# Kernel tuning notes

Hardware: AMD Instinct MI355X
Metric: run time of the kernel (lower is better)

## Reference

```python
import jax, jax.numpy as jnp
import numpy as np
import math

B, S, D, H, DFF, V = 8, 512, 512, 8, 2048, 32000
EPS = 1e-5

def _pe_table(max_len, d):
    pos = jnp.arange(max_len, dtype=jnp.float32)[:, None]
    i = jnp.arange(d)
    exponent = (2 * (i // 2)).astype(jnp.float32) / d
    angle = pos / jnp.power(10000.0, exponent)[None, :]
    return jnp.where(i % 2 == 0, jnp.sin(angle), jnp.cos(angle))

def _ln(x, g, b):
    mu = jnp.mean(x, -1, keepdims=True)
    var = jnp.mean((x - mu) ** 2, -1, keepdims=True)
    return g * (x - mu) * jax.lax.rsqrt(var + EPS) + b

def setup_inputs() -> dict:
    key = jax.random.key(0)
    ks = jax.random.split(key, 16)
    n = jax.random.normal
    return {
        "tokens": jax.random.randint(ks[0], (B, S), 0, V, dtype=jnp.int32),
        "emb": n(ks[1], (V, D), jnp.float32),
        "pe": _pe_table(1000, D),
        "Wq": n(ks[2], (H, D, D), jnp.float32), "bq": jnp.zeros((H, D), jnp.float32),
        "Wk": n(ks[3], (H, D, D), jnp.float32), "bk": jnp.zeros((H, D), jnp.float32),
        "Wv": n(ks[4], (H, D, D), jnp.float32), "bv": jnp.zeros((H, D), jnp.float32),
        "Wo": n(ks[5], (H * D, D), jnp.float32), "bo": jnp.zeros((D,), jnp.float32),
        "g1": jnp.ones((D,), jnp.float32), "be1": jnp.zeros((D,), jnp.float32),
        "W1": n(ks[6], (D, DFF), jnp.float32), "b1": jnp.zeros((DFF,), jnp.float32),
        "W2": n(ks[7], (DFF, D), jnp.float32), "b2": jnp.zeros((D,), jnp.float32),
        "g2": jnp.ones((D,), jnp.float32), "be2": jnp.zeros((D,), jnp.float32),
        "Wf": n(ks[8], (D, V), jnp.float32), "bf": jnp.zeros((V,), jnp.float32),
    }

def reference(tokens, emb, pe, Wq, bq, Wk, bk, Wv, bv, Wo, bo, g1, be1,
              W1, b1, W2, b2, g2, be2, Wf, bf):
    x = emb[tokens] + pe[:tokens.shape[1]]  # [B,S,D]
    res = x
    # input-level "causal" mask over (seq, feature) plane, as in the source
    mask = jnp.triu(jnp.ones((S, D), dtype=bool), k=1)
    xm = jnp.where(mask, 0.0, x)
    scale = 1.0 / math.sqrt(D)
    q = jnp.einsum('bsd,hde->hbse', xm, Wq) + bq[:, None, None, :]
    k = jnp.einsum('bsd,hde->hbse', xm, Wk) + bk[:, None, None, :]
    v = jnp.einsum('bsd,hde->hbse', xm, Wv) + bv[:, None, None, :]
    attn = jax.nn.softmax(jnp.einsum('hbse,hbte->hbst', q, k) * scale, axis=-1)
    o = jnp.einsum('hbst,hbte->hbse', attn, v)  # [H,B,S,D]
    cat = o.transpose(1, 2, 0, 3).reshape(B, S, H * D)  # matches torch.cat head order
    x = _ln(res + (cat @ Wo + bo), g1, be1)
    res = x
    ff = jax.nn.relu(x @ W1 + b1) @ W2 + b2
    x = _ln(res + ff, g2, be2)
    return x @ Wf + bf  # [B,S,V]
```

## Files before the change

kernel.cpp:

```cpp
#include <hip/hip_runtime.h>

typedef unsigned short u16;
typedef unsigned int u32;
typedef short s16x8 __attribute__((ext_vector_type(8)));
typedef __bf16 bf16x8 __attribute__((ext_vector_type(8)));
typedef float f32x4 __attribute__((ext_vector_type(4)));

#define DEVI static __device__ __forceinline__

#define SS 512
#define DD 512
#define NFF 2048
#define VV 32000
#define MTOT 4096
#define HD 4096
#define KC 1536

DEVI float bf2f(u16 h){ return __uint_as_float(((u32)h) << 16); }
DEVI u16 f2bf(float f){
  u32 u = __float_as_uint(f);
  return (u16)((u + 0x7FFFu + ((u >> 16) & 1u)) >> 16);
}
DEVI float ldf(const void* p, long i, int isbf){
  return isbf ? bf2f(((const u16*)p)[i]) : ((const float*)p)[i];
}

DEVI f32x4 mfma16(s16x8 a, s16x8 b, f32x4 c){
  return __builtin_amdgcn_mfma_f32_16x16x32_bf16(
      __builtin_bit_cast(bf16x8, a), __builtin_bit_cast(bf16x8, b), c, 0, 0, 0);
}

typedef const __attribute__((address_space(1))) unsigned int* gup;
typedef __attribute__((address_space(3))) unsigned int* lup;
DEVI void gload16(const void* g, void* l){
  __builtin_amdgcn_global_load_lds((gup)g, (lup)l, 16, 0, 0);
}

DEVI float wave_redsum(float v){
  #pragma unroll
  for (int off = 32; off > 0; off >>= 1) v += __shfl_xor(v, off, 64);
  return v;
}

__global__ void k_dflag(const void* pe, int* flag){
  flag[0] = (*(const u32*)pe == 0x3F800000u) ? 1 : 0;
}

__global__ __launch_bounds__(256) void k_embed(
    const int* __restrict__ tok, const void* __restrict__ emb, const void* __restrict__ pe,
    float* __restrict__ x, u16* __restrict__ xm2, const int* __restrict__ dflag)
{
  int isbf = dflag[0];
  int blk = blockIdx.x;
  int s = blk & (SS - 1);
  int t = tok[blk];
  long rb = (long)blk * 1024;
  for (int d = threadIdx.x; d < DD; d += 256){
    float e = ldf(emb, (long)t * DD + d, isbf) + ldf(pe, (long)s * DD + d, isbf);
    x[(long)blk * DD + d] = e;
    float m = (d <= s) ? e : 0.f;
    u16 hi = f2bf(m);
    u16 lo = f2bf(m - bf2f(hi));
    xm2[rb + d] = hi;
    xm2[rb + 512 + d] = lo;
  }
}

__global__ __launch_bounds__(256) void k_wsplitT(
    const void* __restrict__ Wq, const void* __restrict__ Wk,
    u16* __restrict__ Wq2, u16* __restrict__ Wk2, const int* __restrict__ dflag)
{
  int isbf = dflag[0];
  int zz = blockIdx.z;
  const void* in = (zz < 8) ? Wq : Wk;
  u16* out = (zz < 8) ? Wq2 : Wk2;
  int z = zz & 7;
  long zin = (long)z * DD * DD;
  long zout = (long)z * DD * 1024;
  __shared__ float t[32][33];
  int e0 = blockIdx.x * 32, d0 = blockIdx.y * 32;
  int tx = threadIdx.x & 31, ty = threadIdx.x >> 5;
  #pragma unroll
  for (int i = 0; i < 4; i++){
    int d = ty + i * 8;
    t[d][tx] = ldf(in, zin + (long)(d0 + d) * DD + e0 + tx, isbf);
  }
  __syncthreads();
  #pragma unroll
  for (int i = 0; i < 4; i++){
    int e = ty + i * 8;
    float v = t[tx][e];
    u16 hi = f2bf(v);
    u16 lo = f2bf(v - bf2f(hi));
    long ob = zout + (long)(e0 + e) * 1024 + d0 + tx;
    out[ob] = hi;
    out[ob + 512] = lo;
  }
}

__global__ __launch_bounds__(256) void k_transAll(
    const void* __restrict__ Wv, const void* __restrict__ Wo,
    const void* __restrict__ W1, const void* __restrict__ W2,
    const void* __restrict__ Wf,
    u16* __restrict__ WvT, u16* __restrict__ WoT, u16* __restrict__ W1T,
    u16* __restrict__ W2T, u16* __restrict__ WfT, const int* __restrict__ dflag)
{
  int isbf = dflag[0];
  int f = blockIdx.x;
  const void* in; u16* out; int R, C, gx, loc;
  if (f < 2048)      { in = Wv; out = WvT; R = 512;  C = 512;   gx = 16;   loc = f; }
  else if (f < 4096) { in = Wo; out = WoT; R = 4096; C = 512;   gx = 16;   loc = f - 2048; }
  else if (f < 5120) { in = W1; out = W1T; R = 512;  C = 2048;  gx = 64;   loc = f - 4096; }
  else if (f < 6144) { in = W2; out = W2T; R = 2048; C = 512;   gx = 16;   loc = f - 5120; }
  else               { in = Wf; out = WfT; R = 512;  C = 32000; gx = 1000; loc = f - 6144; }
  int bx = loc % gx;
  int rest = loc / gx;
  int gy = R >> 5;
  int by = rest % gy, z = rest / gy;
  long zo = (long)z * R * C;
  __shared__ float t[32][33];
  int c0 = bx * 32, r0 = by * 32;
  int tx = threadIdx.x & 31, ty = threadIdx.x >> 5;
  #pragma unroll
  for (int i = 0; i < 4; i++){
    int r = ty + i * 8;
    t[r][tx] = ldf(in, zo + (long)(r0 + r) * C + c0 + tx, isbf);
  }
  __syncthreads();
  #pragma unroll
  for (int i = 0; i < 4; i++){
    int c = ty + i * 8;
    out[zo + (long)(c0 + c) * R + r0 + tx] = f2bf(t[tx][c]);
  }
}

enum { EP_QK = 0, EP_SCALE = 1, EP_VT = 2, EP_CAT = 3, EP_OUT = 4,
       EP_F32RES = 5, EP_RELU = 6 };

template<int MODE, bool GSWAP>
__global__ __launch_bounds__(256) void k_mfma(
    const u16* __restrict__ A, long sA, int lda,
    const u16* __restrict__ Bt, long sB,
    void* __restrict__ Cv,
    const void* __restrict__ bias,
    const float* __restrict__ res,
    int K, int ldc, float scale,
    const int* __restrict__ dflag)
{
  int isbf = dflag[0];
  int z = blockIdx.z;
  const u16* Ab = A + (long)z * sA;
  const u16* Bb = Bt + (long)z * sB;
  __shared__ __align__(16) u16 As[2][4][128][8];
  __shared__ __align__(16) u16 Bs[2][4][128][8];
  int m0 = (GSWAP ? blockIdx.x : blockIdx.y) * 128;
  int n0 = (GSWAP ? blockIdx.y : blockIdx.x) * 128;
  int tid = threadIdx.x;
  int lane = tid & 63, w = tid >> 6;
  int wr = (w >> 1) * 64, wc = (w & 1) * 64;
  int l15 = lane & 15, l4 = lane >> 4;
  int s0 = w * 64 + lane;
  int ar0 = s0 & 127, ak0 = s0 >> 7;
  int ak1 = ak0 + 2;
  f32x4 zero = {0.f, 0.f, 0.f, 0.f};
  f32x4 acc[4][4];
  #pragma unroll
  for (int i = 0; i < 4; i++)
    #pragma unroll
    for (int j = 0; j < 4; j++) acc[i][j] = zero;

  const long arow0 = (long)(m0 + ar0) * lda;
  const long brow0 = (long)(n0 + ar0) * K;

  #define STAGE(buf, k0) do{ \
    u16* AsF = &As[buf][0][0][0]; \
    u16* BsF = &Bs[buf][0][0][0]; \
    gload16(Ab + arow0 + (k0) + ak0 * 8, AsF + (long)(w * 64) * 8); \
    gload16(Ab + arow0 + (k0) + ak1 * 8, AsF + (long)(256 + w * 64) * 8); \
    gload16(Bb + brow0 + (k0) + ak0 * 8, BsF + (long)(w * 64) * 8); \
    gload16(Bb + brow0 + (k0) + ak1 * 8, BsF + (long)(256 + w * 64) * 8); \
  }while(0)

  #define COMPUTE(buf) do{ \
    s16x8 af[4], bfr[4]; \
    _Pragma("unroll") \
    for (int i = 0; i < 4; i++) af[i] = *(const s16x8*)&As[buf][l4][wr + i * 16 + l15][0]; \
    _Pragma("unroll") \
    for (int j = 0; j < 4; j++) bfr[j] = *(const s16x8*)&Bs[buf][l4][wc + j * 16 + l15][0]; \
    _Pragma("unroll") \
    for (int i = 0; i < 4; i++) \
      _Pragma("unroll") \
      for (int j = 0; j < 4; j++) \
        acc[i][j] = mfma16(af[i], bfr[j], acc[i][j]); \
  }while(0)

  STAGE(0, 0);
  __syncthreads();
  for (int k0 = 0; k0 < K; k0 += 64){
    STAGE(1, k0 + 32);
    COMPUTE(0);
    __syncthreads();
    if (k0 + 64 < K) STAGE(0, k0 + 64);
    COMPUTE(1);
    __syncthreads();
  }
  #undef STAGE
  #undef COMPUTE

  int mbase = m0 + wr + l4 * 4;
  int nbase = n0 + wc + l15;
  if constexpr (MODE == EP_F32RES){
    float* C = (float*)Cv;
    #pragma unroll
    for (int j = 0; j < 4; j++){
      int n = nbase + j * 16;
      float badd = ldf(bias, n, isbf);
      #pragma unroll
      for (int i = 0; i < 4; i++)
        #pragma unroll
        for (int r = 0; r < 4; r++){
          long a = (long)(mbase + i * 16 + r) * ldc + n;
          C[a] = acc[i][j][r] + badd + res[a];
        }
    }
  } else if constexpr (MODE == EP_RELU){
    u16* C = (u16*)Cv;
    #pragma unroll
    for (int j = 0; j < 4; j++){
      int n = nbase + j * 16;
      float badd = ldf(bias, n, isbf);
      #pragma unroll
      for (int i = 0; i < 4; i++)
        #pragma unroll
        for (int r = 0; r < 4; r++)
          C[(long)(mbase + i * 16 + r) * ldc + n] = f2bf(fmaxf(acc[i][j][r] + badd, 0.f));
    }
  }
}

template<int MODE, bool GSWAP, int AMAP, int BMAP>
__global__ __launch_bounds__(512, 2) void k_mfma2(
    const u16* __restrict__ A, long sA, int lda,
    const u16* __restrict__ Bt, long sB, int ldb,
    void* __restrict__ Cv,
    const void* __restrict__ bias,
    const float* __restrict__ res,
    int K, int ldc, float scale,
    const int* __restrict__ dflag)
{
  int isbf = dflag[0];
  int z = blockIdx.z;
  const u16* Ab = A + (long)z * sA;
  const u16* Bb = Bt + (long)z * sB;
  __shared__ __align__(16) char smem[65536];
  u16* SA = (u16*)smem;
  u16* SB = (u16*)(smem + 32768);
  int m0 = (GSWAP ? blockIdx.x : blockIdx.y) * 256;
  int n0 = (GSWAP ? blockIdx.y : blockIdx.x) * 256;
  int tid = threadIdx.x;
  int lane = tid & 63, w = tid >> 6;
  int wm = (w >> 2) * 128, wn = (w & 3) * 64;
  int l15 = lane & 15, l4 = lane >> 4;
  int row = tid & 255, ob = tid >> 8;
  f32x4 zero = {0.f, 0.f, 0.f, 0.f};
  f32x4 acc[8][4];
  #pragma unroll
  for (int i = 0; i < 8; i++)
    #pragma unroll
    for (int j = 0; j < 4; j++) acc[i][j] = zero;

  const long arow0 = (long)(m0 + row) * lda;
  const long brow0 = (long)(n0 + row) * ldb;

  #define STAGE2(buf, k0_) do{ \
    int ka = (AMAP == 1) ? ((k0_) < 512 ? (k0_) : (k0_) - 512) \
           : (AMAP == 2) ? ((k0_) < 1024 ? (k0_) : (k0_) - 1024) : (k0_); \
    int kb = (BMAP == 1) ? ((k0_) < 512 ? (k0_) : (k0_) - 512) \
           : (BMAP == 2) ? ((k0_) < 1024 ? (k0_) : (k0_) - 1024) : (k0_); \
    gload16(Ab + arow0 + ka + ob * 8,       SA + ((buf) * 8192 + (ob * 256 + row) * 8)); \
    gload16(Ab + arow0 + ka + (ob + 2) * 8, SA + ((buf) * 8192 + ((ob + 2) * 256 + row) * 8)); \
    gload16(Bb + brow0 + kb + ob * 8,       SB + ((buf) * 8192 + (ob * 256 + row) * 8)); \
    gload16(Bb + brow0 + kb + (ob + 2) * 8, SB + ((buf) * 8192 + ((ob + 2) * 256 + row) * 8)); \
  }while(0)

  #define COMPUTE2(buf) do{ \
    s16x8 bfr[4]; \
    _Pragma("unroll") \
    for (int j = 0; j < 4; j++) \
      bfr[j] = *(const s16x8*)(SB + ((buf) * 8192 + l4 * 2048 + (wn + j * 16 + l15) * 8)); \
    _Pragma("unroll") \
    for (int i = 0; i < 8; i++){ \
      s16x8 af = *(const s16x8*)(SA + ((buf) * 8192 + l4 * 2048 + (wm + i * 16 + l15) * 8)); \
      _Pragma("unroll") \
      for (int j = 0; j < 4; j++) \
        acc[i][j] = mfma16(af, bfr[j], acc[i][j]); \
    } \
  }while(0)

  STAGE2(0, 0);
  __syncthreads();
  for (int k0 = 0; k0 < K; k0 += 64){
    STAGE2(1, k0 + 32);
    COMPUTE2(0);
    __syncthreads();
    if (k0 + 64 < K) STAGE2(0, k0 + 64);
    COMPUTE2(1);
    __syncthreads();
  }
  #undef STAGE2
  #undef COMPUTE2

  int mbase = m0 + wm + l4 * 4;
  int nbase = n0 + wn + l15;
  if constexpr (MODE == EP_CAT){
    u16* C = (u16*)Cv;
    int h = z >> 3, b = z & 7;
    #pragma unroll
    for (int i = 0; i < 8; i++){
      int s = mbase + i * 16;
      #pragma unroll
      for (int j = 0; j < 4; j++){
        int n = nbase + j * 16;
        #pragma unroll
        for (int r = 0; r < 4; r++)
          C[((long)b * SS + s + r) * HD + (long)h * DD + n] = f2bf(acc[i][j][r]);
      }
    }
  } else if constexpr (MODE == EP_OUT){
    float* O = (float*)Cv;
    float* ldsT = (float*)smem;
    const int RST = 260;
    int hs16 = (w >> 2) * 16;
    float badd[4];
    #pragma unroll
    for (int j = 0; j < 4; j++) badd[j] = ldf(bias, n0 + wn + j * 16 + l15, isbf);
    #pragma unroll
    for (int i = 0; i < 8; i++){
      __syncthreads();
      #pragma unroll
      for (int j = 0; j < 4; j++){
        int col = wn + j * 16 + l15;
        #pragma unroll
        for (int r = 0; r < 4; r++)
          ldsT[(hs16 + l4 * 4 + r) * RST + col] = acc[i][j][r] + badd[j];
      }
      __syncthreads();
      #pragma unroll
      for (int p = 0; p < 4; p++){
        int chunk = tid + p * 512;
        int lr = chunk >> 6, c4 = chunk & 63;
        int gm = m0 + (lr >> 4) * 128 + i * 16 + (lr & 15);
        f32x4 v = *(f32x4*)&ldsT[lr * RST + c4 * 4];
        __builtin_nontemporal_store(v, (f32x4*)&O[(long)gm * ldc + n0 + c4 * 4]);
      }
    }
  }
}

__global__ __launch_bounds__(512, 2) void k_proj(
    const u16* __restrict__ xm2,
    const u16* __restrict__ Wq2, const u16* __restrict__ Wk2, const u16* __restrict__ WvT,
    u16* __restrict__ q2, u16* __restrict__ k2, u16* __restrict__ vT,
    const void* __restrict__ bq, const void* __restrict__ bk, const void* __restrict__ bv,
    const int* __restrict__ dflag)
{
  int isbf = dflag[0];
  int zz = blockIdx.z;
  int z, ldb, K, amap, bmap, mode;
  const u16* Bb; const void* bias; u16* C;
  if (zz < 16){
    mode = 0; z = zz & 7;
    Bb = (zz < 8 ? Wq2 : Wk2) + (long)z * 524288;
    ldb = 1024; K = KC; amap = 1; bmap = 2;
    bias = (zz < 8) ? bq : bk;
    C = (zz < 8) ? q2 : k2;
  } else {
    mode = 1; z = zz - 16;
    Bb = WvT + (long)z * 262144;
    ldb = 512; K = 512; amap = 0; bmap = 0;
    bias = bv;
    C = vT;
  }
  const u16* Ab = xm2;
  __shared__ __align__(16) char smem[65536];
  u16* SA = (u16*)smem;
  u16* SB = (u16*)(smem + 32768);
  int m0 = blockIdx.y * 256;
  int n0 = blockIdx.x * 256;
  int tid = threadIdx.x;
  int lane = tid & 63, w = tid >> 6;
  int wm = (w >> 2) * 128, wn = (w & 3) * 64;
  int l15 = lane & 15, l4 = lane >> 4;
  int row = tid & 255, ob = tid >> 8;
  f32x4 zero = {0.f, 0.f, 0.f, 0.f};
  f32x4 acc[8][4];
  #pragma unroll
  for (int i = 0; i < 8; i++)
    #pragma unroll
    for (int j = 0; j < 4; j++) acc[i][j] = zero;

  const long arow0 = (long)(m0 + row) * 1024;
  const long brow0 = (long)(n0 + row) * ldb;

  #define STAGEP(buf, k0_) do{ \
    int ka = (amap == 1) ? ((k0_) < 512 ? (k0_) : (k0_) - 512) : (k0_); \
    int kb = (bmap == 2) ? ((k0_) < 1024 ? (k0_) : (k0_) - 1024) : (k0_); \
    gload16(Ab + arow0 + ka + ob * 8,       SA + ((buf) * 8192 + (ob * 256 + row) * 8)); \
    gload16(Ab + arow0 + ka + (ob + 2) * 8, SA + ((buf) * 8192 + ((ob + 2) * 256 + row) * 8)); \
    gload16(Bb + brow0 + kb + ob * 8,       SB + ((buf) * 8192 + (ob * 256 + row) * 8)); \
    gload16(Bb + brow0 + kb + (ob + 2) * 8, SB + ((buf) * 8192 + ((ob + 2) * 256 + row) * 8)); \
  }while(0)

  #define COMPUTEP(buf) do{ \
    s16x8 bfr[4]; \
    _Pragma("unroll") \
    for (int j = 0; j < 4; j++) \
      bfr[j] = *(const s16x8*)(SB + ((buf) * 8192 + l4 * 2048 + (wn + j * 16 + l15) * 8)); \
    _Pragma("unroll") \
    for (int i = 0; i < 8; i++){ \
      s16x8 af = *(const s16x8*)(SA + ((buf) * 8192 + l4 * 2048 + (wm + i * 16 + l15) * 8)); \
      _Pragma("unroll") \
      for (int j = 0; j < 4; j++) \
        acc[i][j] = mfma16(af, bfr[j], acc[i][j]); \
    } \
  }while(0)

  STAGEP(0, 0);
  __syncthreads();
  for (int k0 = 0; k0 < K; k0 += 64){
    STAGEP(1, k0 + 32);
    COMPUTEP(0);
    __syncthreads();
    if (k0 + 64 < K) STAGEP(0, k0 + 64);
    COMPUTEP(1);
    __syncthreads();
  }
  #undef STAGEP
  #undef COMPUTEP

  int mbase = m0 + wm + l4 * 4;
  int nbase = n0 + wn + l15;
  if (mode == 0){
    u16* Cz = C + (long)z * ((long)MTOT * 1024);
    #pragma unroll
    for (int j = 0; j < 4; j++){
      int n = nbase + j * 16;
      float badd = ldf(bias, (long)z * DD + n, isbf);
      #pragma unroll
      for (int i = 0; i < 8; i++)
        #pragma unroll
        for (int r = 0; r < 4; r++){
          float qv = acc[i][j][r] + badd;
          u16 hi = f2bf(qv);
          u16 lo = f2bf(qv - bf2f(hi));
          long rb = (long)(mbase + i * 16 + r) * 1024;
          Cz[rb + n] = hi;
          Cz[rb + 512 + n] = lo;
        }
    }
  } else {
    #pragma unroll
    for (int i = 0; i < 8; i++){
      int mrow = mbase + i * 16;
      int b = mrow >> 9, s = mrow & (SS - 1);
      #pragma unroll
      for (int j = 0; j < 4; j++){
        int n = nbase + j * 16;
        float badd = ldf(bias, (long)z * DD + n, isbf);
        ushort4 pk;
        pk.x = f2bf(acc[i][j][0] + badd); pk.y = f2bf(acc[i][j][1] + badd);
        pk.z = f2bf(acc[i][j][2] + badd); pk.w = f2bf(acc[i][j][3] + badd);
        *(ushort4*)&C[((long)(z * 8 + b) * DD + n) * SS + s] = pk;
      }
    }
  }
}

template<int AMAP, int BMAP>
__global__ __launch_bounds__(512, 2) void k_fsm(
    const u16* __restrict__ A, long sA, int lda,
    const u16* __restrict__ Bt, long sB, int ldb,
    u16* __restrict__ P, int K, float scale,
    const int* __restrict__ dflag)
{
  int z = blockIdx.z;
  const u16* Ab = A + (long)z * sA;
  const u16* Bb = Bt + (long)z * sB;
  __shared__ __align__(16) char smem[81920];
  u16* SA = (u16*)smem;
  u16* SB = (u16*)(smem + 16384);
  int m0 = blockIdx.x * 128;
  int tid = threadIdx.x;
  int lane = tid & 63, w = tid >> 6;
  int wn = w * 64;
  int l15 = lane & 15, l4 = lane >> 4;
  f32x4 zero = {0.f, 0.f, 0.f, 0.f};
  f32x4 acc[8][4];
  #pragma unroll
  for (int i = 0; i < 8; i++)
    #pragma unroll
    for (int j = 0; j < 4; j++) acc[i][j] = zero;

  const long arow0 = (long)(m0 + (tid & 127)) * lda;
  const int akc = tid >> 7;
  const long brow0 = (long)tid * ldb;

  #define STAGEF(buf, k0_) do{ \
    int ka = (AMAP == 1) ? ((k0_) < 512 ? (k0_) : (k0_) - 512) \
           : (AMAP == 2) ? ((k0_) < 1024 ? (k0_) : (k0_) - 1024) : (k0_); \
    int kb = (BMAP == 1) ? ((k0_) < 512 ? (k0_) : (k0_) - 512) \
           : (BMAP == 2) ? ((k0_) < 1024 ? (k0_) : (k0_) - 1024) : (k0_); \
    gload16(Ab + arow0 + ka + akc * 8, SA + ((buf) * 4096 + tid * 8)); \
    gload16(Bb + brow0 + kb + 0,  SB + ((buf) * 16384 + (0 * 512 + tid) * 8)); \
    gload16(Bb + brow0 + kb + 8,  SB + ((buf) * 16384 + (1 * 512 + tid) * 8)); \
    gload16(Bb + brow0 + kb + 16, SB + ((buf) * 16384 + (2 * 512 + tid) * 8)); \
    gload16(Bb + brow0 + kb + 24, SB + ((buf) * 16384 + (3 * 512 + tid) * 8)); \
  }while(0)

  #define COMPUTEF(buf) do{ \
    s16x8 bfr[4]; \
    _Pragma("unroll") \
    for (int j = 0; j < 4; j++) \
      bfr[j] = *(const s16x8*)(SB + ((buf) * 16384 + l4 * 4096 + (wn + j * 16 + l15) * 8)); \
    _Pragma("unroll") \
    for (int i = 0; i < 8; i++){ \
      s16x8 af = *(const s16x8*)(SA + ((buf) * 4096 + l4 * 1024 + (i * 16 + l15) * 8)); \
      _Pragma("unroll") \
      for (int j = 0; j < 4; j++) \
        acc[i][j] = mfma16(af, bfr[j], acc[i][j]); \
    } \
  }while(0)

  STAGEF(0, 0);
  __syncthreads();
  for (int k0 = 0; k0 < K; k0 += 64){
    STAGEF(1, k0 + 32);
    COMPUTEF(0);
    __syncthreads();
    if (k0 + 64 < K) STAGEF(0, k0 + 64);
    COMPUTEF(1);
    __syncthreads();
  }
  #undef STAGEF
  #undef COMPUTEF

  float* sred = (float*)smem;
  float* srow = (float*)(smem + 4096);

  #pragma unroll
  for (int i = 0; i < 8; i++)
    #pragma unroll
    for (int j = 0; j < 4; j++)
      acc[i][j] *= scale;

  #pragma unroll
  for (int i = 0; i < 8; i++)
    #pragma unroll
    for (int r = 0; r < 4; r++){
      float m = fmaxf(fmaxf(acc[i][0][r], acc[i][1][r]),
                      fmaxf(acc[i][2][r], acc[i][3][r]));
      #pragma unroll
      for (int off = 1; off < 16; off <<= 1) m = fmaxf(m, __shfl_xor(m, off, 64));
      if (l15 == 0) sred[w * 128 + l4 * 4 + i * 16 + r] = m;
    }
  __syncthreads();
  if (tid < 128){
    float m = sred[tid];
    #pragma unroll
    for (int w2 = 1; w2 < 8; w2++) m = fmaxf(m, sred[w2 * 128 + tid]);
    srow[tid] = m;
  }
  __syncthreads();
  #pragma unroll
  for (int i = 0; i < 8; i++)
    #pragma unroll
    for (int r = 0; r < 4; r++){
      float rm = srow[l4 * 4 + i * 16 + r];
      float s = 0.f;
      #pragma unroll
      for (int j = 0; j < 4; j++){
        float e = expf(acc[i][j][r] - rm);
        acc[i][j][r] = e;
        s += e;
      }
      #pragma unroll
      for (int off = 1; off < 16; off <<= 1) s += __shfl_xor(s, off, 64);
      if (l15 == 0) sred[w * 128 + l4 * 4 + i * 16 + r] = s;
    }
  __syncthreads();
  if (tid < 128){
    float s = 0.f;
    #pragma unroll
    for (int w2 = 0; w2 < 8; w2++) s += sred[w2 * 128 + tid];
    srow[tid] = 1.f / s;
  }
  __syncthreads();
  u16* Pz = P + (long)z * ((long)SS * SS);
  #pragma unroll
  for (int i = 0; i < 8; i++)
    #pragma unroll
    for (int r = 0; r < 4; r++){
      int rl = l4 * 4 + i * 16 + r;
      float inv = srow[rl];
      long rb = (long)(m0 + rl) * SS;
      #pragma unroll
      for (int j = 0; j < 4; j++)
        Pz[rb + wn + j * 16 + l15] = f2bf(acc[i][j][r] * inv);
    }
}

template<bool WF32>
__global__ __launch_bounds__(256) void k_ln(
    const float* __restrict__ X, const void* __restrict__ g, const void* __restrict__ be,
    u16* __restrict__ Yb, float* __restrict__ Yf, const int* __restrict__ dflag)
{
  int isbf = dflag[0];
  int row = blockIdx.x * 4 + (threadIdx.x >> 6);
  int lane = threadIdx.x & 63;
  const float* p = X + (long)row * DD + lane * 8;
  float4 v0 = *(const float4*)p;
  float4 v1 = *(const float4*)(p + 4);
  float v[8] = {v0.x, v0.y, v0.z, v0.w, v1.x, v1.y, v1.z, v1.w};
  float s = 0.f;
  #pragma unroll
  for (int i = 0; i < 8; i++) s += v[i];
  s = wave_redsum(s);
  float mu = s * (1.f / DD);
  float d_[8], sq = 0.f;
  #pragma unroll
  for (int i = 0; i < 8; i++){ d_[i] = v[i] - mu; sq += d_[i] * d_[i]; }
  sq = wave_redsum(sq);
  float rs = 1.f / sqrtf(sq * (1.f / DD) + 1e-5f);
  #pragma unroll
  for (int i = 0; i < 8; i++){
    int dd = lane * 8 + i;
    float y = ldf(g, dd, isbf) * d_[i] * rs + ldf(be, dd, isbf);
    Yb[(long)row * DD + dd] = f2bf(y);
    if (WF32) Yf[(long)row * DD + dd] = y;
  }
}

extern "C" void kernel_launch(void* const* d_in, const int* in_sizes, int n_in,
                              void* d_out, int out_size, void* d_ws, size_t ws_size,
                              hipStream_t stream)
{
  const int* tokens = (const int*)d_in[0];
  const void* emb = d_in[1];
  const void* pe  = d_in[2];
  const void* Wq  = d_in[3];
  const void* bq  = d_in[4];
  const void* Wk  = d_in[5];
  const void* bk  = d_in[6];
  const void* Wv  = d_in[7];
  const void* bv  = d_in[8];
  const void* Wo  = d_in[9];
  const void* bo  = d_in[10];
  const void* g1  = d_in[11];
  const void* be1 = d_in[12];
  const void* W1  = d_in[13];
  const void* b1  = d_in[14];
  const void* W2  = d_in[15];
  const void* b2  = d_in[16];
  const void* g2  = d_in[17];
  const void* be2 = d_in[18];
  const void* Wf  = d_in[19];
  const void* bfb = d_in[20];
  float* out = (float*)d_out;
  char* ws = (char*)d_ws;
  char* DO = (char*)d_out;

  const size_t MB = 1ull << 20;
  int* dflag = (int*)ws;
  u16* x2b   = (u16*)(ws + 1 * MB);
  u16* WfT   = (u16*)(ws + 8 * MB);

  float* x    = (float*)(DO + 0 * MB);
  u16*   xm2  = (u16*)(DO + 8 * MB);
  u16*   Wq2  = (u16*)(DO + 16 * MB);
  u16*   Wk2  = (u16*)(DO + 24 * MB);
  u16*   WvT  = (u16*)(DO + 32 * MB);
  u16*   WoT  = (u16*)(DO + 36 * MB);
  u16*   W1T  = (u16*)(DO + 40 * MB);
  u16*   W2T  = (u16*)(DO + 42 * MB);
  u16*   q2   = (u16*)(DO + 48 * MB);
  u16*   k2   = (u16*)(DO + 112 * MB);
  u16*   attn = (u16*)(DO + 240 * MB);
  u16*   vT   = (u16*)(DO + 272 * MB);
  u16*   cat  = (u16*)(DO + 304 * MB);
  float* proj = (float*)(DO + 336 * MB);
  float* x1f  = (float*)(DO + 344 * MB);
  u16*   x1b  = (u16*)(DO + 352 * MB);
  u16*   ff1  = (u16*)(DO + 356 * MB);
  float* ff2  = (float*)(DO + 372 * MB);

  const float scale = 0.04419417382415922f;
  const long HSL = 262144;
  const long QSL = 524288;

  k_dflag<<<1, 1, 0, stream>>>(pe, dflag);
  k_embed<<<dim3(4096), 256, 0, stream>>>(tokens, emb, pe, x, xm2, dflag);

  k_wsplitT<<<dim3(16, 16, 16), 256, 0, stream>>>(Wq, Wk, Wq2, Wk2, dflag);
  k_transAll<<<dim3(22144), 256, 0, stream>>>(
      Wv, Wo, W1, W2, Wf, WvT, WoT, W1T, W2T, WfT, dflag);

  k_proj<<<dim3(2, 16, 24), 512, 0, stream>>>(
      xm2, Wq2, Wk2, WvT, q2, k2, vT, bq, bk, bv, dflag);

  k_fsm<1, 2><<<dim3(4, 1, 64), 512, 0, stream>>>(
      q2, QSL, 1024, k2, QSL, 1024, attn, KC, scale, dflag);

  k_mfma2<EP_CAT, false, 0, 0><<<dim3(2, 2, 64), 512, 0, stream>>>(
      attn, HSL, SS, vT, HSL, 512, cat, nullptr, nullptr, SS, 0, 0.f, dflag);

  k_mfma<EP_F32RES, false><<<dim3(4, 32, 1), 256, 0, stream>>>(
      cat, 0, HD, WoT, 0, proj, bo, x, HD, DD, 0.f, dflag);
  k_ln<true><<<dim3(1024), 256, 0, stream>>>(proj, g1, be1, x1b, x1f, dflag);

  k_mfma<EP_RELU, false><<<dim3(16, 32, 1), 256, 0, stream>>>(
      x1b, 0, DD, W1T, 0, ff1, b1, nullptr, DD, NFF, 0.f, dflag);
  k_mfma<EP_F32RES, false><<<dim3(4, 32, 1), 256, 0, stream>>>(
      ff1, 0, NFF, W2T, 0, ff2, b2, x1f, NFF, DD, 0.f, dflag);
  k_ln<false><<<dim3(1024), 256, 0, stream>>>(ff2, g2, be2, x2b, nullptr, dflag);

  k_mfma2<EP_OUT, true, 0, 0><<<dim3(16, 125, 1), 512, 0, stream>>>(
      x2b, 0, DD, WfT, 0, 512, out, bfb, nullptr, DD, VV, 0.f, dflag);
}
```

Baseline: 994.6 us.

## Stage softmax P tiles through LDS for coalesced stores and swizzle GEMM block order

The softmax kernel's probability output now goes through a padded shared-memory buffer, 32 rows at a time, before being written to global memory as 8-byte vectors across full rows. Previously each lane scattered 2-byte stores. Separately, the GSWAP GEMM variant remaps its linear block index into eight interleaved groups to change which tiles run concurrently, aiming for better L2/cache locality. The staging adds extra barriers and LDS traffic, and the remap assumes the grid size is divisible by eight.

After: 1.003 ms. About the same (+0.8%).

```diff
diff --git a/kernel.cpp b/kernel.cpp
--- a/kernel.cpp
+++ b/kernel.cpp
@@ -255,8 +255,17 @@
   __shared__ __align__(16) char smem[65536];
   u16* SA = (u16*)smem;
   u16* SB = (u16*)(smem + 32768);
-  int m0 = (GSWAP ? blockIdx.x : blockIdx.y) * 256;
-  int n0 = (GSWAP ? blockIdx.y : blockIdx.x) * 256;
+  int m0, n0;
+  if constexpr (GSWAP){
+    int f = blockIdx.x + gridDim.x * blockIdx.y;
+    int q = (gridDim.x * gridDim.y) >> 3;
+    int L = (f & 7) * q + (f >> 3);
+    m0 = (L % gridDim.x) * 256;
+    n0 = (L / gridDim.x) * 256;
+  } else {
+    m0 = blockIdx.y * 256;
+    n0 = blockIdx.x * 256;
+  }
   int tid = threadIdx.x;
   int lane = tid & 63, w = tid >> 6;
   int wm = (w >> 2) * 128, wn = (w & 3) * 64;
@@ -596,17 +605,32 @@
   }
   __syncthreads();
   u16* Pz = P + (long)z * ((long)SS * SS);
-  #pragma unroll
-  for (int i = 0; i < 8; i++)
-    #pragma unroll
-    for (int r = 0; r < 4; r++){
-      int rl = l4 * 4 + i * 16 + r;
-      float inv = srow[rl];
-      long rb = (long)(m0 + rl) * SS;
-      #pragma unroll
-      for (int j = 0; j < 4; j++)
-        Pz[rb + wn + j * 16 + l15] = f2bf(acc[i][j][r] * inv);
-    }
+  u16* pb = (u16*)(smem + 8192);
+  const int PST = 520;
+  #pragma unroll
+  for (int ii = 0; ii < 4; ii++){
+    __syncthreads();
+    #pragma unroll
+    for (int s2 = 0; s2 < 2; s2++){
+      int i = ii * 2 + s2;
+      #pragma unroll
+      for (int r = 0; r < 4; r++){
+        int rl = l4 * 4 + i * 16 + r;
+        float inv = srow[rl];
+        #pragma unroll
+        for (int j = 0; j < 4; j++)
+          pb[(s2 * 16 + l4 * 4 + r) * PST + wn + j * 16 + l15] = f2bf(acc[i][j][r] * inv);
+      }
+    }
+    __syncthreads();
+    #pragma unroll
+    for (int p = 0; p < 8; p++){
+      int chunk = tid + p * 512;
+      int lr = chunk >> 7, c8 = chunk & 127;
+      ushort4 v = *(ushort4*)&pb[lr * PST + c8 * 4];
+      *(ushort4*)&Pz[(long)(m0 + ii * 32 + lr) * SS + c8 * 4] = v;
+    }
+  }
 }
 
 template<bool WF32>
```
